# Optimization experiments

Measured on AMD Instinct MI355X. Metric: run time of the kernel, lower is better.

## Reference

```python
import jax, jax.numpy as jnp
import numpy as np

N_NODES = 50000
N_EDGES = 400000
IN_DIM = 128
HIDDEN = 128
OUT_DIM = 128
MIX = 4

def _gelu(x):
    return jax.nn.gelu(x, approximate=False)  # torch default erf-GELU

def setup_inputs() -> dict:
    key = jax.random.key(0)
    ks = jax.random.split(key, 8)
    X = jax.random.normal(ks[0], (N_NODES, IN_DIM), dtype=jnp.float32)
    edge_index = jax.random.randint(ks[1], (2, N_EDGES), 0, N_NODES, dtype=jnp.int64)
    s = lambda fan_in: 1.0 / np.sqrt(fan_in)
    W1 = jax.random.uniform(ks[2], (HIDDEN, IN_DIM), jnp.float32, -s(IN_DIM), s(IN_DIM))
    b1 = jax.random.uniform(ks[3], (HIDDEN,), jnp.float32, -s(IN_DIM), s(IN_DIM))
    WA = jax.random.uniform(ks[4], (HIDDEN, HIDDEN), jnp.float32, -s(HIDDEN), s(HIDDEN))
    WB = jax.random.uniform(ks[5], (MIX, HIDDEN), jnp.float32, -s(HIDDEN), s(HIDDEN))
    W2 = jax.random.uniform(ks[6], (OUT_DIM, 2 * HIDDEN), jnp.float32, -s(2 * HIDDEN), s(2 * HIDDEN))
    b2 = jax.random.uniform(ks[7], (OUT_DIM,), jnp.float32, -s(2 * HIDDEN), s(2 * HIDDEN))
    return {"X": X, "edge_index": edge_index, "W1": W1, "b1": b1,
            "WA": WA, "WB": WB, "W2": W2, "b2": b2}

def reference(X, edge_index, W1, b1, WA, WB, W2, b2):
    num_nodes = X.shape[0]
    # ff1 -> gelu (dropout identity in eval)
    H = _gelu(X @ W1.T + b1)                       # (N, h)
    src, dst = edge_index[0], edge_index[1]
    X_src = H[src]                                 # (E, h) gather
    # hyper target weights per edge
    W_tar = _gelu(X_src @ WA.T) @ WB.T             # (E, m)
    # per-edge outer product, scatter_add over dst
    cross = X_src[:, :, None] * W_tar[:, None, :]  # (E, h, m)
    agg = jax.ops.segment_sum(cross, dst, num_segments=num_nodes)  # (N, h, m)
    agg = _gelu(agg)
    # gather back per edge, contract mix dim
    out_edge = jnp.einsum('ehm,em->eh', agg[dst], W_tar)  # (E, h)
    # scatter_mean over dst
    ones = jnp.ones((src.shape[0],), X.dtype)
    cnt = jax.ops.segment_sum(ones, dst, num_segments=num_nodes)   # (N,)
    agg_node = jax.ops.segment_sum(out_edge, dst, num_segments=num_nodes)
    agg_node = agg_node / jnp.maximum(cnt, 1.0)[:, None]           # (N, h)
    # root connection + gelu, ff2
    feat = _gelu(jnp.concatenate([agg_node, H], axis=1))           # (N, 2h)
    out = feat @ W2.T + b2                                          # (N, out)
    return out
```

## Files before the change

### kernel.cpp

```cpp
#include <hip/hip_runtime.h>
#include <hip/hip_bf16.h>

#define NN 50000
#define NE 400000
#define NT 3125

typedef unsigned short u16;
typedef short short8 __attribute__((ext_vector_type(8)));
typedef float f32x4 __attribute__((ext_vector_type(4)));

__device__ __forceinline__ float geluf(float x){ return 0.5f*x*(1.0f+erff(x*0.70710678118654752440f)); }
__device__ __forceinline__ u16 f2bfb(float f){
  union { __hip_bfloat16 h; u16 u; } cv; cv.h = __float2bfloat16(f); return cv.u;
}
__device__ __forceinline__ float bfb2f(u16 u){ return __uint_as_float(((unsigned)u)<<16); }

__global__ __launch_bounds__(256) void k_pre(const float* __restrict__ W1,
    const float* __restrict__ WA, const float* __restrict__ W2,
    u16* __restrict__ W1b, u16* __restrict__ WAb, u16* __restrict__ W2b,
    const int* __restrict__ dst, int* __restrict__ deg)
{
  if (blockIdx.x < 64){
    int i4 = (blockIdx.x*256 + threadIdx.x) * 4;
    const float* srcp; u16* dstp; int off;
    if (i4 < 16384){ srcp = W1; dstp = W1b; off = i4; }
    else if (i4 < 32768){ srcp = WA; dstp = WAb; off = i4 - 16384; }
    else { srcp = W2; dstp = W2b; off = i4 - 32768; }
    float4 v = *(const float4*)(srcp + off);
    ushort4 o;
    o.x = f2bfb(v.x); o.y = f2bfb(v.y); o.z = f2bfb(v.z); o.w = f2bfb(v.w);
    *(ushort4*)(dstp + off) = o;
  } else {
    int e = (blockIdx.x - 64)*256 + threadIdx.x;
    if (e < NE) atomicAdd(&deg[dst[e]], 1);
  }
}

__global__ __launch_bounds__(512) void k_ff1(const float* __restrict__ X,
    const u16* __restrict__ W1b, const float* __restrict__ b1,
    u16* __restrict__ Hb, u16* __restrict__ GHb)
{
  extern __shared__ u16 wls[];
  const int LDW = 136;
  for (int idx8 = threadIdx.x*8; idx8 < 128*128; idx8 += 512*8){
    int c = idx8 >> 7, k = idx8 & 127;
    *(short8*)&wls[c*LDW + k] = *(const short8*)(W1b + idx8);
  }
  __syncthreads();
  const int lane = threadIdx.x & 63;
  const int wave = threadIdx.x >> 6;
  const int lrow = lane & 15;
  const int kgrp = lane >> 4;
  float4 b1v[8];
  #pragma unroll
  for (int nb = 0; nb < 8; nb++) b1v[nb] = *(const float4*)(b1 + nb*16 + kgrp*4);
  for (int tile = blockIdx.x*8 + wave; tile < NT; tile += gridDim.x*8){
    const float* xr = X + (size_t)(tile*16 + lrow)*128 + kgrp*8;
    f32x4 acc[8];
    #pragma unroll
    for (int nb = 0; nb < 8; nb++) acc[nb] = (f32x4){0.f,0.f,0.f,0.f};
    #pragma unroll
    for (int kk = 0; kk < 4; kk++){
      float4 xa = *(const float4*)(xr + kk*32);
      float4 xb = *(const float4*)(xr + kk*32 + 4);
      union { short8 v; u16 u[8]; } af;
      af.u[0]=f2bfb(xa.x); af.u[1]=f2bfb(xa.y); af.u[2]=f2bfb(xa.z); af.u[3]=f2bfb(xa.w);
      af.u[4]=f2bfb(xb.x); af.u[5]=f2bfb(xb.y); af.u[6]=f2bfb(xb.z); af.u[7]=f2bfb(xb.w);
      #pragma unroll
      for (int nb = 0; nb < 8; nb++){
        short8 bf = *(const short8*)&wls[(nb*16 + lrow)*LDW + kk*32 + kgrp*8];
        acc[nb] = __builtin_amdgcn_mfma_f32_16x16x32_bf16(bf, af.v, acc[nb], 0, 0, 0);
      }
    }
    const size_t rb = (size_t)(tile*16 + lrow)*128 + kgrp*4;
    #pragma unroll
    for (int nb = 0; nb < 8; nb++){
      ushort4 hp, gp;
      #pragma unroll
      for (int r = 0; r < 4; r++){
        float h = geluf(acc[nb][r] + b1v[nb][r]);
        ((u16*)&hp)[r] = f2bfb(h);
        ((u16*)&gp)[r] = f2bfb(geluf(h));
      }
      *(ushort4*)(Hb  + rb + nb*16) = hp;
      *(ushort4*)(GHb + rb + nb*16) = gp;
    }
  }
}

__global__ __launch_bounds__(1024) void k_scan(const int* __restrict__ deg, int* __restrict__ offs){
  __shared__ int wsum[16];
  __shared__ int sbase_s;
  const int tid = threadIdx.x, lane = tid & 63, wave = tid >> 6;
  if (tid == 0) sbase_s = 0;
  __syncthreads();
  for (int base = 0; base < NN; base += 4096){
    int i0 = base + tid*4;
    int v0=0,v1=0,v2=0,v3=0;
    if (i0+3 < NN){ int4 v = *(const int4*)(deg+i0); v0=v.x;v1=v.y;v2=v.z;v3=v.w; }
    else {
      if (i0   < NN) v0 = deg[i0];
      if (i0+1 < NN) v1 = deg[i0+1];
      if (i0+2 < NN) v2 = deg[i0+2];
    }
    int own = v0+v1+v2+v3;
    int inc = own;
    #pragma unroll
    for (int s=1;s<64;s<<=1){ int t = __shfl_up(inc, s, 64); if (lane >= s) inc += t; }
    if (lane == 63) wsum[wave] = inc;
    __syncthreads();
    if (wave == 0 && lane < 16){
      int w = wsum[lane];
      #pragma unroll
      for (int s=1;s<16;s<<=1){ int t = __shfl_up(w, s, 64); if (lane >= s) w += t; }
      wsum[lane] = w;
    }
    __syncthreads();
    int sbase = sbase_s;
    int wbase = sbase + (wave ? wsum[wave-1] : 0);
    int excl = wbase + inc - own;
    if (i0   < NN) offs[i0]   = excl;
    if (i0+1 < NN) offs[i0+1] = excl + v0;
    if (i0+2 < NN) offs[i0+2] = excl + v0+v1;
    if (i0+3 < NN) offs[i0+3] = excl + v0+v1+v2;
    __syncthreads();
    if (tid == 0) sbase_s = sbase + wsum[15];
    __syncthreads();
  }
  if (tid == 0) offs[NN] = sbase_s;
}

__global__ void k_fill(const int* __restrict__ src, const int* __restrict__ dst,
                       const int* __restrict__ offs, int* __restrict__ cur,
                       int* __restrict__ slist){
  int e = blockIdx.x*256 + threadIdx.x;
  if (e < NE){
    int d = dst[e];
    int p = atomicAdd(&cur[d], 1);
    slist[offs[d] + p] = src[e];
  }
}

__global__ __launch_bounds__(512) void k_node(const u16* __restrict__ Hb,
    const u16* __restrict__ WAb, const float* __restrict__ WB,
    float* __restrict__ T)
{
  extern __shared__ u16 was[];
  const int LDW = 136;
  for (int idx8 = threadIdx.x*8; idx8 < 128*128; idx8 += 512*8){
    int h = idx8 >> 7, k = idx8 & 127;
    *(short8*)&was[h*LDW + k] = *(const short8*)(WAb + idx8);
  }
  const int lane = threadIdx.x & 63;
  const int wave = threadIdx.x >> 6;
  const int lrow = lane & 15;
  const int kgrp = lane >> 4;
  float wbv[4][8];
  #pragma unroll
  for (int m = 0; m < 4; m++)
    #pragma unroll
    for (int nb = 0; nb < 8; nb++)
      wbv[m][nb] = WB[m*128 + nb*16 + lrow];
  __syncthreads();
  for (int tile = blockIdx.x*8 + wave; tile < NT; tile += gridDim.x*8){
    const u16* hr = Hb + (size_t)(tile*16 + lrow)*128 + kgrp*8;
    f32x4 acc[8];
    #pragma unroll
    for (int nb = 0; nb < 8; nb++) acc[nb] = (f32x4){0.f,0.f,0.f,0.f};
    #pragma unroll
    for (int kk = 0; kk < 4; kk++){
      short8 af = *(const short8*)(hr + kk*32);
      #pragma unroll
      for (int nb = 0; nb < 8; nb++){
        short8 bf = *(const short8*)&was[(nb*16 + lrow)*LDW + kk*32 + kgrp*8];
        acc[nb] = __builtin_amdgcn_mfma_f32_16x16x32_bf16(af, bf, acc[nb], 0, 0, 0);
      }
    }
    float part[4][4];
    #pragma unroll
    for (int r = 0; r < 4; r++)
      #pragma unroll
      for (int m = 0; m < 4; m++) part[r][m] = 0.f;
    #pragma unroll
    for (int nb = 0; nb < 8; nb++){
      float g0 = geluf(acc[nb][0]), g1 = geluf(acc[nb][1]);
      float g2 = geluf(acc[nb][2]), g3 = geluf(acc[nb][3]);
      #pragma unroll
      for (int m = 0; m < 4; m++){
        float w = wbv[m][nb];
        part[0][m] += g0*w; part[1][m] += g1*w;
        part[2][m] += g2*w; part[3][m] += g3*w;
      }
    }
    #pragma unroll
    for (int s = 1; s < 16; s <<= 1)
      #pragma unroll
      for (int r = 0; r < 4; r++)
        #pragma unroll
        for (int m = 0; m < 4; m++)
          part[r][m] += __shfl_xor(part[r][m], s, 64);
    if (lrow == 0){
      #pragma unroll
      for (int r = 0; r < 4; r++){
        f32x4 tv = { part[r][0], part[r][1], part[r][2], part[r][3] };
        *(f32x4*)&T[(size_t)(tile*16 + kgrp*4 + r)*4] = tv;
      }
    }
  }
}

__global__ __launch_bounds__(256) void k_agg(const u16* __restrict__ Hb,
    const float* __restrict__ T, const int* __restrict__ offs,
    const int* __restrict__ slist, u16* __restrict__ GAb)
{
  const int lane = threadIdx.x & 63;
  const int wave = threadIdx.x >> 6;
  const int vo = lane*2;
  for (int v = blockIdx.x*4 + wave; v < NN; v += gridDim.x*4){
    const int e0 = __builtin_amdgcn_readfirstlane(offs[v]);
    const int e1 = __builtin_amdgcn_readfirstlane(offs[v+1]);
    float ax0=0, ax1=0, ax2=0, ax3=0;
    float ay0=0, ay1=0, ay2=0, ay3=0;
    float s0=0, s1=0, s2=0, s3=0;
    int idx = e0;
    for (; idx + 8 <= e1; idx += 8){
      unsigned pk[8]; float4 tt[8];
      #pragma unroll
      for (int u = 0; u < 8; u++){
        int sn = slist[idx+u];
        pk[u] = *(const unsigned*)(Hb + (size_t)sn*128 + vo);
        tt[u] = *(const float4*)(T + (size_t)sn*4);
      }
      #pragma unroll
      for (int u = 0; u < 8; u++){
        float hx = bfb2f((u16)(pk[u] & 0xffffu));
        float hy = bfb2f((u16)(pk[u] >> 16));
        ax0 += hx*tt[u].x; ax1 += hx*tt[u].y; ax2 += hx*tt[u].z; ax3 += hx*tt[u].w;
        ay0 += hy*tt[u].x; ay1 += hy*tt[u].y; ay2 += hy*tt[u].z; ay3 += hy*tt[u].w;
        s0 += tt[u].x; s1 += tt[u].y; s2 += tt[u].z; s3 += tt[u].w;
      }
    }
    for (; idx + 4 <= e1; idx += 4){
      unsigned pk[4]; float4 tt[4];
      #pragma unroll
      for (int u = 0; u < 4; u++){
        int sn = slist[idx+u];
        pk[u] = *(const unsigned*)(Hb + (size_t)sn*128 + vo);
        tt[u] = *(const float4*)(T + (size_t)sn*4);
      }
      #pragma unroll
      for (int u = 0; u < 4; u++){
        float hx = bfb2f((u16)(pk[u] & 0xffffu));
        float hy = bfb2f((u16)(pk[u] >> 16));
        ax0 += hx*tt[u].x; ax1 += hx*tt[u].y; ax2 += hx*tt[u].z; ax3 += hx*tt[u].w;
        ay0 += hy*tt[u].x; ay1 += hy*tt[u].y; ay2 += hy*tt[u].z; ay3 += hy*tt[u].w;
        s0 += tt[u].x; s1 += tt[u].y; s2 += tt[u].z; s3 += tt[u].w;
      }
    }
    for (; idx < e1; idx++){
      int sn = slist[idx];
      unsigned pk = *(const unsigned*)(Hb + (size_t)sn*128 + vo);
      float hx = bfb2f((u16)(pk & 0xffffu));
      float hy = bfb2f((u16)(pk >> 16));
      float4 wt = *(const float4*)(T + (size_t)sn*4);
      ax0 += hx*wt.x; ax1 += hx*wt.y; ax2 += hx*wt.z; ax3 += hx*wt.w;
      ay0 += hy*wt.x; ay1 += hy*wt.y; ay2 += hy*wt.z; ay3 += hy*wt.w;
      s0 += wt.x; s1 += wt.y; s2 += wt.z; s3 += wt.w;
    }
    float inv = 1.0f / fmaxf((float)(e1 - e0), 1.0f);
    float ox = geluf(ax0)*s0 + geluf(ax1)*s1 + geluf(ax2)*s2 + geluf(ax3)*s3;
    float oy = geluf(ay0)*s0 + geluf(ay1)*s1 + geluf(ay2)*s2 + geluf(ay3)*s3;
    ushort2 res;
    res.x = f2bfb(geluf(ox * inv));
    res.y = f2bfb(geluf(oy * inv));
    *(ushort2*)(GAb + (size_t)v*128 + vo) = res;
  }
}

__global__ __launch_bounds__(512) void k_ff2(const u16* __restrict__ GAb,
    const u16* __restrict__ GHb, const u16* __restrict__ W2b,
    const float* __restrict__ b2, float* __restrict__ out)
{
  extern __shared__ u16 w2s[];
  const int LDW = 264;
  for (int idx8 = threadIdx.x*8; idx8 < 128*256; idx8 += 512*8){
    int o = idx8 >> 8, k = idx8 & 255;
    *(short8*)&w2s[o*LDW + k] = *(const short8*)(W2b + idx8);
  }
  __syncthreads();
  const int lane = threadIdx.x & 63;
  const int wave = threadIdx.x >> 6;
  const int lrow = lane & 15;
  const int kgrp = lane >> 4;
  float4 b2v[8];
  #pragma unroll
  for (int nb = 0; nb < 8; nb++) b2v[nb] = *(const float4*)(b2 + nb*16 + kgrp*4);
  for (int tile = blockIdx.x*8 + wave; tile < NT; tile += gridDim.x*8){
    const int row = tile*16 + lrow;
    const u16* aga = GAb + (size_t)row*128 + kgrp*8;
    const u16* agh = GHb + (size_t)row*128 + kgrp*8;
    f32x4 acc[8];
    #pragma unroll
    for (int nb = 0; nb < 8; nb++) acc[nb] = (f32x4){0.f,0.f,0.f,0.f};
    #pragma unroll
    for (int kk = 0; kk < 8; kk++){
      short8 af = (kk < 4) ? *(const short8*)(aga + kk*32)
                           : *(const short8*)(agh + (kk-4)*32);
      #pragma unroll
      for (int nb = 0; nb < 8; nb++){
        short8 bf = *(const short8*)&w2s[(nb*16 + lrow)*LDW + kk*32 + kgrp*8];
        acc[nb] = __builtin_amdgcn_mfma_f32_16x16x32_bf16(bf, af, acc[nb], 0, 0, 0);
      }
    }
    float* orp = out + (size_t)row*128 + kgrp*4;
    #pragma unroll
    for (int nb = 0; nb < 8; nb++){
      f32x4 o;
      o[0] = acc[nb][0] + b2v[nb].x;
      o[1] = acc[nb][1] + b2v[nb].y;
      o[2] = acc[nb][2] + b2v[nb].z;
      o[3] = acc[nb][3] + b2v[nb].w;
      *(f32x4*)(orp + nb*16) = o;
    }
  }
}

extern "C" void kernel_launch(void* const* d_in, const int* in_sizes, int n_in,
                              void* d_out, int out_size, void* d_ws, size_t ws_size,
                              hipStream_t stream)
{
  (void)in_sizes; (void)n_in; (void)out_size; (void)ws_size;
  const float* X  = (const float*)d_in[0];
  const int*   ei = (const int*)d_in[1];
  const float* W1 = (const float*)d_in[2];
  const float* b1 = (const float*)d_in[3];
  const float* WA = (const float*)d_in[4];
  const float* WB = (const float*)d_in[5];
  const float* W2 = (const float*)d_in[6];
  const float* b2 = (const float*)d_in[7];
  float* out = (float*)d_out;
  const int* src = ei;
  const int* dst = ei + NE;

  char* p = (char*)d_ws;
  u16*   Hb   = (u16*)(p);
  u16*   GHb  = (u16*)(p + 12800000);
  u16*   GAb  = (u16*)(p + 25600000);
  float* T    = (float*)(p + 38400000);
  int*   deg  = (int*)(p + 39200000);
  int*   cur  = (int*)(p + 39400192);
  int*   offs = (int*)(p + 39600384);
  int*   slist= (int*)(p + 39800832);
  u16*   W1b  = (u16*)(p + 41400832);
  u16*   WAb  = (u16*)(p + 41433600);
  u16*   W2b  = (u16*)(p + 41466368);

  (void)hipMemsetAsync(deg, 0, 400384, stream);

  (void)hipFuncSetAttribute((const void*)k_ff2, hipFuncAttributeMaxDynamicSharedMemorySize, 128*264*2);

  k_pre <<<64 + (NE+255)/256, 256, 0, stream>>>(W1, WA, W2, W1b, WAb, W2b, dst, deg);
  k_ff1 <<<391, 512, 128*136*2, stream>>>(X, W1b, b1, Hb, GHb);
  k_scan<<<1, 1024, 0, stream>>>(deg, offs);
  k_fill<<<(NE+255)/256, 256, 0, stream>>>(src, dst, offs, cur, slist);
  k_node<<<391, 512, 128*136*2, stream>>>(Hb, WAb, WB, T);
  k_agg <<<2048, 256, 0, stream>>>(Hb, T, offs, slist, GAb);
  k_ff2 <<<391, 512, 128*264*2, stream>>>(GAb, GHb, W2b, b2, out);
}
```

Measured before the change: 171.5 us.

## Recompute GELU(H) in ff2 instead of storing GH; change tile mapping and grid

Stops writing the separate GELU(H) buffer in ff1 and recomputes GELU on the fly from H when ff2 loads the root-connection half of its input. This removes a 12.8 MB write and a 12.8 MB read in exchange for extra erf work in ff2. Tiles are now assigned to waves in a strided interleaved order, and the grids of ff1, node and ff2 grow from 391 to 512 blocks. Recomputing from bf16 H may give rounding slightly different from the stored bf16 GH.

```diff
diff --git a/kernel.cpp b/kernel.cpp
--- a/kernel.cpp
+++ b/kernel.cpp
@@ -38,7 +38,7 @@
 
 __global__ __launch_bounds__(512) void k_ff1(const float* __restrict__ X,
     const u16* __restrict__ W1b, const float* __restrict__ b1,
-    u16* __restrict__ Hb, u16* __restrict__ GHb)
+    u16* __restrict__ Hb)
 {
   extern __shared__ u16 wls[];
   const int LDW = 136;
@@ -54,7 +54,7 @@
   float4 b1v[8];
   #pragma unroll
   for (int nb = 0; nb < 8; nb++) b1v[nb] = *(const float4*)(b1 + nb*16 + kgrp*4);
-  for (int tile = blockIdx.x*8 + wave; tile < NT; tile += gridDim.x*8){
+  for (int tile = wave*gridDim.x + blockIdx.x; tile < NT; tile += gridDim.x*8){
     const float* xr = X + (size_t)(tile*16 + lrow)*128 + kgrp*8;
     f32x4 acc[8];
     #pragma unroll
@@ -75,15 +75,11 @@
     const size_t rb = (size_t)(tile*16 + lrow)*128 + kgrp*4;
     #pragma unroll
     for (int nb = 0; nb < 8; nb++){
-      ushort4 hp, gp;
-      #pragma unroll
-      for (int r = 0; r < 4; r++){
-        float h = geluf(acc[nb][r] + b1v[nb][r]);
-        ((u16*)&hp)[r] = f2bfb(h);
-        ((u16*)&gp)[r] = f2bfb(geluf(h));
-      }
-      *(ushort4*)(Hb  + rb + nb*16) = hp;
-      *(ushort4*)(GHb + rb + nb*16) = gp;
+      ushort4 hp;
+      #pragma unroll
+      for (int r = 0; r < 4; r++)
+        ((u16*)&hp)[r] = f2bfb(geluf(acc[nb][r] + b1v[nb][r]));
+      *(ushort4*)(Hb + rb + nb*16) = hp;
     }
   }
 }
@@ -162,7 +158,7 @@
     for (int nb = 0; nb < 8; nb++)
       wbv[m][nb] = WB[m*128 + nb*16 + lrow];
   __syncthreads();
-  for (int tile = blockIdx.x*8 + wave; tile < NT; tile += gridDim.x*8){
+  for (int tile = wave*gridDim.x + blockIdx.x; tile < NT; tile += gridDim.x*8){
     const u16* hr = Hb + (size_t)(tile*16 + lrow)*128 + kgrp*8;
     f32x4 acc[8];
     #pragma unroll
@@ -278,7 +274,7 @@
 }
 
 __global__ __launch_bounds__(512) void k_ff2(const u16* __restrict__ GAb,
-    const u16* __restrict__ GHb, const u16* __restrict__ W2b,
+    const u16* __restrict__ Hb, const u16* __restrict__ W2b,
     const float* __restrict__ b2, float* __restrict__ out)
 {
   extern __shared__ u16 w2s[];
@@ -295,17 +291,26 @@
   float4 b2v[8];
   #pragma unroll
   for (int nb = 0; nb < 8; nb++) b2v[nb] = *(const float4*)(b2 + nb*16 + kgrp*4);
-  for (int tile = blockIdx.x*8 + wave; tile < NT; tile += gridDim.x*8){
+  for (int tile = wave*gridDim.x + blockIdx.x; tile < NT; tile += gridDim.x*8){
     const int row = tile*16 + lrow;
     const u16* aga = GAb + (size_t)row*128 + kgrp*8;
-    const u16* agh = GHb + (size_t)row*128 + kgrp*8;
+    const u16* agh = Hb  + (size_t)row*128 + kgrp*8;
     f32x4 acc[8];
     #pragma unroll
     for (int nb = 0; nb < 8; nb++) acc[nb] = (f32x4){0.f,0.f,0.f,0.f};
     #pragma unroll
     for (int kk = 0; kk < 8; kk++){
-      short8 af = (kk < 4) ? *(const short8*)(aga + kk*32)
-                           : *(const short8*)(agh + (kk-4)*32);
+      short8 af;
+      if (kk < 4){
+        af = *(const short8*)(aga + kk*32);
+      } else {
+        short8 hb = *(const short8*)(agh + (kk-4)*32);
+        union { short8 v; u16 u[8]; } g;
+        #pragma unroll
+        for (int j = 0; j < 8; j++)
+          g.u[j] = f2bfb(geluf(bfb2f(((const u16*)&hb)[j])));
+        af = g.v;
+      }
       #pragma unroll
       for (int nb = 0; nb < 8; nb++){
         short8 bf = *(const short8*)&w2s[(nb*16 + lrow)*LDW + kk*32 + kgrp*8];
@@ -344,26 +349,25 @@
 
   char* p = (char*)d_ws;
   u16*   Hb   = (u16*)(p);
-  u16*   GHb  = (u16*)(p + 12800000);
-  u16*   GAb  = (u16*)(p + 25600000);
-  float* T    = (float*)(p + 38400000);
-  int*   deg  = (int*)(p + 39200000);
-  int*   cur  = (int*)(p + 39400192);
-  int*   offs = (int*)(p + 39600384);
-  int*   slist= (int*)(p + 39800832);
-  u16*   W1b  = (u16*)(p + 41400832);
-  u16*   WAb  = (u16*)(p + 41433600);
-  u16*   W2b  = (u16*)(p + 41466368);
+  u16*   GAb  = (u16*)(p + 12800000);
+  float* T    = (float*)(p + 25600000);
+  int*   deg  = (int*)(p + 26400000);
+  int*   cur  = (int*)(p + 26600192);
+  int*   offs = (int*)(p + 26800384);
+  int*   slist= (int*)(p + 27000832);
+  u16*   W1b  = (u16*)(p + 28600832);
+  u16*   WAb  = (u16*)(p + 28633600);
+  u16*   W2b  = (u16*)(p + 28666368);
 
   (void)hipMemsetAsync(deg, 0, 400384, stream);
 
   (void)hipFuncSetAttribute((const void*)k_ff2, hipFuncAttributeMaxDynamicSharedMemorySize, 128*264*2);
 
   k_pre <<<64 + (NE+255)/256, 256, 0, stream>>>(W1, WA, W2, W1b, WAb, W2b, dst, deg);
-  k_ff1 <<<391, 512, 128*136*2, stream>>>(X, W1b, b1, Hb, GHb);
+  k_ff1 <<<512, 512, 128*136*2, stream>>>(X, W1b, b1, Hb);
   k_scan<<<1, 1024, 0, stream>>>(deg, offs);
   k_fill<<<(NE+255)/256, 256, 0, stream>>>(src, dst, offs, cur, slist);
-  k_node<<<391, 512, 128*136*2, stream>>>(Hb, WAb, WB, T);
+  k_node<<<512, 512, 128*136*2, stream>>>(Hb, WAb, WB, T);
   k_agg <<<2048, 256, 0, stream>>>(Hb, T, offs, slist, GAb);
-  k_ff2 <<<391, 512, 128*264*2, stream>>>(GAb, GHb, W2b, b2, out);
-}
+  k_ff2 <<<512, 512, 128*264*2, stream>>>(GAb, Hb, W2b, b2, out);
+}
```

After: 171.7 us. No clear change (+0.1%).
